# Optimization experiments

Measured on AMD Instinct MI355X. Metric: run time of the kernel, lower is better.

The kernel has to match this reference:

```python
import jax, jax.numpy as jnp
import numpy as np

N = 16384
IN_FEATS = 128
HIDDEN = 128
OUT_FEATS = 64


def setup_inputs() -> dict:
    key = jax.random.key(0)
    ks = jax.random.split(key, 8)
    x = jax.random.normal(ks[0], (N, IN_FEATS), dtype=jnp.float32)
    adj = jax.random.uniform(ks[1], (N, N), dtype=jnp.float32)
    def glorot(k, shape):
        lim = 1.0 / np.sqrt(shape[0])
        return jax.random.uniform(k, shape, minval=-lim, maxval=lim, dtype=jnp.float32)
    W1 = glorot(ks[2], (IN_FEATS, HIDDEN))
    b1 = jnp.zeros((HIDDEN,), dtype=jnp.float32)
    W2 = glorot(ks[3], (HIDDEN, OUT_FEATS))
    b2 = jnp.zeros((OUT_FEATS,), dtype=jnp.float32)
    W_out = glorot(ks[4], (OUT_FEATS, 1))
    b_out = jnp.zeros((1,), dtype=jnp.float32)
    return {"x": x, "adj": adj, "W1": W1, "b1": b1, "W2": W2, "b2": b2,
            "W_out": W_out, "b_out": b_out}


def _gcn_layer(x, adj, W, b):
    # support = x @ W ; out = adj @ support + b  (standard GraphConvLayer)
    return adj @ (x @ W) + b


def reference(x, adj, W1, b1, W2, b2, W_out, b_out):
    h = jax.nn.relu(_gcn_layer(x, adj, W1, b1))      # [N, hidden]
    h = _gcn_layer(h, adj, W2, b2)                   # [N, out_feats]
    pooled = h.sum(axis=0)                           # [out_feats] graph readout
    return pooled @ W_out + b_out                    # [1]
```

## Files before the change

kernel.cpp:

```cpp
#include <hip/hip_runtime.h>
#include <hip/hip_bf16.h>
#include <stdint.h>

#define NN   16384
#define FI   128
#define FH   128
#define FO   64

#define BM   32
#define BK   64
#define LDK  72
#define NT   (NN / BK)
#define NPART 2048

typedef float f32x4 __attribute__((ext_vector_type(4)));
typedef short s16x8 __attribute__((ext_vector_type(8)));
typedef short s16x4 __attribute__((ext_vector_type(4)));

__device__ __forceinline__ unsigned short f2bf(float f) {
    union { float f; unsigned u; } v; v.f = f;
    unsigned u = v.u;
    return (unsigned short)((u + 0x7FFFu + ((u >> 16) & 1u)) >> 16);
}

__global__ __launch_bounds__(256) void k1_s1t(const float* __restrict__ x,
                                              const float* __restrict__ W1,
                                              unsigned short* __restrict__ S1T) {
    __shared__ float w1s[FI][FH];
    __shared__ float xs[64][132];

    const int t  = threadIdx.x;
    const int b  = blockIdx.x;
    const int k0 = b * 64;

    float* wflat = &w1s[0][0];
    for (int i = t; i < FI * FH; i += 256) wflat[i] = W1[i];

    #pragma unroll
    for (int s = 0; s < 8; ++s) {
        int idx = t + 256 * s;
        int r   = idx >> 5;
        int f4  = idx & 31;
        f32x4 vv = *(const f32x4*)(x + (size_t)(k0 + r) * FI + f4 * 4);
        *(f32x4*)(&xs[r][f4 * 4]) = vv;
    }
    __syncthreads();

    const int w = t >> 6;
    const int l = t & 63;

    float acc[32];
    #pragma unroll
    for (int j = 0; j < 32; ++j) acc[j] = 0.f;

    for (int f4 = 0; f4 < 32; ++f4) {
        f32x4 xv = *(const f32x4*)(&xs[l][f4 * 4]);
        #pragma unroll
        for (int e = 0; e < 4; ++e) {
            const int f = f4 * 4 + e;
            #pragma unroll
            for (int cth = 0; cth < 8; ++cth) {
                f32x4 wv = *(const f32x4*)(&w1s[f][w * 32 + cth * 4]);
                acc[cth * 4 + 0] += xv[e] * wv[0];
                acc[cth * 4 + 1] += xv[e] * wv[1];
                acc[cth * 4 + 2] += xv[e] * wv[2];
                acc[cth * 4 + 3] += xv[e] * wv[3];
            }
        }
    }

    const int k = k0 + l;
    #pragma unroll
    for (int j = 0; j < 32; ++j) {
        const int n = w * 32 + j;
        S1T[(size_t)n * NN + k] = f2bf(acc[j]);
    }
}

__global__ __launch_bounds__(256, 2) void k2_agg(const float* __restrict__ adj,
                                                 const unsigned short* __restrict__ S1T,
                                                 float* __restrict__ T,
                                                 float* __restrict__ cpart) {
    __shared__ unsigned short aA[2][BM][LDK];
    __shared__ unsigned short bB[2][FH][LDK];

    const int  t    = threadIdx.x;
    const long m0   = (long)blockIdx.x * BM;
    const int  w    = t >> 6;
    const int  l    = t & 63;
    const int  ar   = t >> 4;
    const int  ac4  = t & 15;
    const int  sn   = t >> 3;
    const int  sch  = t & 7;
    const int  m    = l & 15;
    const int  quad = l >> 4;

    f32x4 acc[2][2];
    #pragma unroll
    for (int i = 0; i < 2; ++i)
        #pragma unroll
        for (int j = 0; j < 2; ++j) acc[i][j] = (f32x4){0.f, 0.f, 0.f, 0.f};

    f32x4 paA0, paA1, paB0, paB1;
    s16x8 psA[4], psB[4];

#define SYNC() do {                                                               \
    asm volatile("s_waitcnt lgkmcnt(0)" ::: "memory");                            \
    __builtin_amdgcn_s_barrier();                                                 \
} while (0)

#define LOAD_TILE(PA0, PA1, PS, KT) do {                                          \
    const long koff_ = (long)(KT) * BK;                                           \
    PA0 = *(const f32x4*)(adj + (m0 + ar) * NN + koff_ + ac4 * 4);                \
    PA1 = *(const f32x4*)(adj + (m0 + ar + 16) * NN + koff_ + ac4 * 4);           \
    _Pragma("unroll")                                                             \
    for (int s_ = 0; s_ < 4; ++s_)                                                \
        PS[s_] = *(const s16x8*)(S1T + (size_t)(sn + 32 * s_) * NN + koff_ + sch * 8); \
} while (0)

#define STAGE(SB, PA0, PA1, PS, KCOL) do {                                        \
    s16x4 q0_, q1_;                                                               \
    _Pragma("unroll")                                                             \
    for (int j_ = 0; j_ < 4; ++j_) {                                              \
        q0_[j_] = (short)f2bf(PA0[j_]);                                           \
        q1_[j_] = (short)f2bf(PA1[j_]);                                           \
    }                                                                             \
    *(s16x4*)(&aA[SB][ar][ac4 * 4])      = q0_;                                   \
    *(s16x4*)(&aA[SB][ar + 16][ac4 * 4]) = q1_;                                   \
    _Pragma("unroll")                                                             \
    for (int s_ = 0; s_ < 4; ++s_)                                                \
        *(s16x8*)(&bB[SB][sn + 32 * s_][sch * 8]) = PS[s_];                       \
      \
      \
      \
    f32x4 pv_;                                                                    \
    _Pragma("unroll")                                                             \
    for (int j_ = 0; j_ < 4; ++j_) {                                              \
        float p_ = PA0[j_] + PA1[j_];                                             \
        p_ += __shfl_xor(p_, 16);                                                 \
        p_ += __shfl_xor(p_, 32);                                                 \
        pv_[j_] = p_;                                                             \
    }                                                                             \
    if (l < 16)                                                                   \
        *(f32x4*)(&cpart[((size_t)blockIdx.x * 4 + w) * NN + (KCOL) + l * 4]) = pv_; \
} while (0)

#define COMPUTE(SB) do {                                                          \
    _Pragma("unroll")                                                             \
    for (int ks = 0; ks < 2; ++ks) {                                              \
        s16x8 af_[2], bf_[2];                                                     \
        _Pragma("unroll")                                                         \
        for (int mt = 0; mt < 2; ++mt)                                            \
            af_[mt] = *(const s16x8*)(&aA[SB][mt * 16 + m][ks * 32 + quad * 8]);  \
        _Pragma("unroll")                                                         \
        for (int nt = 0; nt < 2; ++nt)                                            \
            bf_[nt] = *(const s16x8*)(&bB[SB][w * 32 + nt * 16 + m][ks * 32 + quad * 8]); \
        _Pragma("unroll")                                                         \
        for (int mt = 0; mt < 2; ++mt)                                            \
            _Pragma("unroll")                                                     \
            for (int nt = 0; nt < 2; ++nt)                                        \
                acc[mt][nt] = __builtin_amdgcn_mfma_f32_16x16x32_bf16(            \
                    af_[mt], bf_[nt], acc[mt][nt], 0, 0, 0);                      \
    }                                                                             \
} while (0)

    LOAD_TILE(paA0, paA1, psA, 0);
    LOAD_TILE(paB0, paB1, psB, 1);
    STAGE(0, paA0, paA1, psA, 0);
    SYNC();

    for (int kt2 = 0; kt2 < NT; kt2 += 2) {
        if (kt2 + 2 < NT) LOAD_TILE(paA0, paA1, psA, kt2 + 2);
        COMPUTE(0);
        STAGE(1, paB0, paB1, psB, (kt2 + 1) * BK);
        SYNC();

        if (kt2 + 3 < NT) LOAD_TILE(paB0, paB1, psB, kt2 + 3);
        COMPUTE(1);
        if (kt2 + 2 < NT) STAGE(0, paA0, paA1, psA, (kt2 + 2) * BK);
        SYNC();
    }

#undef LOAD_TILE
#undef STAGE
#undef COMPUTE
#undef SYNC

    #pragma unroll
    for (int mt = 0; mt < 2; ++mt)
        #pragma unroll
        for (int nt = 0; nt < 2; ++nt) {
            const int col = w * 32 + nt * 16 + m;
            #pragma unroll
            for (int r = 0; r < 4; ++r) {
                const long row = m0 + mt * 16 + quad * 4 + r;
                T[row * FH + col] = acc[mt][nt][r];
            }
        }
}

__global__ __launch_bounds__(256) void k3_v(const float* __restrict__ T,
                                            const float* __restrict__ cpart,
                                            const float* __restrict__ b1,
                                            float* __restrict__ v) {
    __shared__ float vp[FH];
    __shared__ float cw[4][64];
    __shared__ float cloc[64];

    const int t = threadIdx.x;
    const int b = blockIdx.x;
    const int w = t >> 6;
    const int l = t & 63;

    float s = 0.f;
    #pragma unroll 8
    for (int i = 0; i < NPART / 4; ++i)
        s += cpart[(size_t)(w + 4 * i) * NN + b * 64 + l];
    cw[w][l] = s;
    if (t < FH) vp[t] = 0.f;
    __syncthreads();
    if (t < 64) cloc[t] = cw[0][t] + cw[1][t] + cw[2][t] + cw[3][t];
    __syncthreads();

    const int kk = t >> 2;
    const int mq = t & 3;
    const int k  = b * 64 + kk;
    const float ck = cloc[kk];

    #pragma unroll
    for (int j4 = 0; j4 < 8; ++j4) {
        f32x4 tv = *(const f32x4*)(T + (size_t)k * FH + mq * 32 + j4 * 4);
        f32x4 bv = *(const f32x4*)(b1 + mq * 32 + j4 * 4);
        #pragma unroll
        for (int e = 0; e < 4; ++e) {
            float h = tv[e] + bv[e];
            h = h > 0.f ? h : 0.f;
            atomicAdd(&vp[mq * 32 + j4 * 4 + e], ck * h);
        }
    }
    __syncthreads();
    if (t < FH) atomicAdd(&v[t], vp[t]);
}

__global__ void k4_out(const float* __restrict__ v, const float* __restrict__ W2,
                       const float* __restrict__ b2, const float* __restrict__ Wout,
                       const float* __restrict__ bout, float* __restrict__ out) {
    const int j = threadIdx.x;
    float pj = (float)NN * b2[j];
    for (int mm = 0; mm < FH; ++mm) pj += v[mm] * W2[mm * FO + j];
    float s = pj * Wout[j];
    #pragma unroll
    for (int off = 32; off; off >>= 1) s += __shfl_down(s, off);
    if (j == 0) out[0] = s + bout[0];
}

extern "C" void kernel_launch(void* const* d_in, const int* in_sizes, int n_in,
                              void* d_out, int out_size, void* d_ws, size_t ws_size,
                              hipStream_t stream) {
    const float* x    = (const float*)d_in[0];
    const float* adj  = (const float*)d_in[1];
    const float* W1   = (const float*)d_in[2];
    const float* b1   = (const float*)d_in[3];
    const float* W2   = (const float*)d_in[4];
    const float* b2   = (const float*)d_in[5];
    const float* Wout = (const float*)d_in[6];
    const float* bout = (const float*)d_in[7];
    float* out = (float*)d_out;

    char* ws = (char*)d_ws;
    unsigned short* S1T = (unsigned short*)ws;
    float* T     = (float*)(ws + (4u   << 20));
    float* cpart = (float*)(ws + (12u  << 20));
    float* v     = (float*)(ws + (140u << 20));

    hipMemsetAsync(v, 0, 512, stream);

    k1_s1t<<<256, 256, 0, stream>>>(x, W1, S1T);
    k2_agg<<<512, 256, 0, stream>>>(adj, S1T, T, cpart);
    k3_v  <<<256, 256, 0, stream>>>(T, cpart, b1, v);
    k4_out<<<1, 64, 0, stream>>>(v, W2, b2, Wout, bout, out);
}
```

Measured before the change: 1.527 ms.

## Halve aggregation row tile, load S1T fragments directly into registers, reduce column partials in LDS

The adjacency aggregation kernel moves from 32-row to 16-row tiles, doubling the grid to 1024 blocks and raising the occupancy hint to 4. Each wave now loads its bf16 S1T MFMA fragments straight from global memory into registers, so the LDS staging buffer for S1T is gone. The per-wave column-sum partials are combined in LDS and written once per block, which halves the cpart array. The cost is that the S1T operand is now fetched once per 16 rows instead of once per 32, doubling its global/L2 traffic.

```diff
diff --git a/kernel.cpp b/kernel.cpp
--- a/kernel.cpp
+++ b/kernel.cpp
@@ -7,11 +7,12 @@
 #define FH   128
 #define FO   64
 
-#define BM   32
+#define BM   16
 #define BK   64
 #define LDK  72
 #define NT   (NN / BK)
-#define NPART 2048
+#define NBLK (NN / BM)
+#define NPART NBLK
 
 typedef float f32x4 __attribute__((ext_vector_type(4)));
 typedef short s16x8 __attribute__((ext_vector_type(8)));
@@ -77,12 +78,12 @@
     }
 }
 
-__global__ __launch_bounds__(256, 2) void k2_agg(const float* __restrict__ adj,
+__global__ __launch_bounds__(256, 4) void k2_agg(const float* __restrict__ adj,
                                                  const unsigned short* __restrict__ S1T,
                                                  float* __restrict__ T,
                                                  float* __restrict__ cpart) {
     __shared__ unsigned short aA[2][BM][LDK];
-    __shared__ unsigned short bB[2][FH][LDK];
+    __shared__ float cs[2][4][BK];
 
     const int  t    = threadIdx.x;
     const long m0   = (long)blockIdx.x * BM;
@@ -90,113 +91,107 @@
     const int  l    = t & 63;
     const int  ar   = t >> 4;
     const int  ac4  = t & 15;
-    const int  sn   = t >> 3;
-    const int  sch  = t & 7;
     const int  m    = l & 15;
     const int  quad = l >> 4;
 
-    f32x4 acc[2][2];
-    #pragma unroll
-    for (int i = 0; i < 2; ++i)
-        #pragma unroll
-        for (int j = 0; j < 2; ++j) acc[i][j] = (f32x4){0.f, 0.f, 0.f, 0.f};
-
-    f32x4 paA0, paA1, paB0, paB1;
-    s16x8 psA[4], psB[4];
+    f32x4 acc[2];
+    acc[0] = (f32x4){0.f, 0.f, 0.f, 0.f};
+    acc[1] = (f32x4){0.f, 0.f, 0.f, 0.f};
+
+    f32x4 paA, paB;
+    s16x8 bfA[2][2], bfB[2][2];
 
 #define SYNC() do {                                                               \
     asm volatile("s_waitcnt lgkmcnt(0)" ::: "memory");                            \
     __builtin_amdgcn_s_barrier();                                                 \
 } while (0)
 
-#define LOAD_TILE(PA0, PA1, PS, KT) do {                                          \
-    const long koff_ = (long)(KT) * BK;                                           \
-    PA0 = *(const f32x4*)(adj + (m0 + ar) * NN + koff_ + ac4 * 4);                \
-    PA1 = *(const f32x4*)(adj + (m0 + ar + 16) * NN + koff_ + ac4 * 4);           \
-    _Pragma("unroll")                                                             \
-    for (int s_ = 0; s_ < 4; ++s_)                                                \
-        PS[s_] = *(const s16x8*)(S1T + (size_t)(sn + 32 * s_) * NN + koff_ + sch * 8); \
-} while (0)
-
-#define STAGE(SB, PA0, PA1, PS, KCOL) do {                                        \
-    s16x4 q0_, q1_;                                                               \
+#define LOADA(PA, KT)                                                             \
+    PA = *(const f32x4*)(adj + (m0 + ar) * NN + (long)(KT) * BK + ac4 * 4)
+
+#define LOADB(BF, KT) do {                                                        \
+    const long ko_ = (long)(KT) * BK;                                             \
+    _Pragma("unroll")                                                             \
+    for (int nt_ = 0; nt_ < 2; ++nt_)                                             \
+        _Pragma("unroll")                                                         \
+        for (int ks_ = 0; ks_ < 2; ++ks_)                                         \
+            BF[nt_][ks_] = *(const s16x8*)(                                       \
+                S1T + (size_t)(w * 32 + nt_ * 16 + m) * NN + ko_ + ks_ * 32 + quad * 8); \
+} while (0)
+
+#define STAGE(SB, PA) do {                                                        \
+    s16x4 q_;                                                                     \
+    _Pragma("unroll")                                                             \
+    for (int j_ = 0; j_ < 4; ++j_) q_[j_] = (short)f2bf(PA[j_]);                  \
+    *(s16x4*)(&aA[SB][ar][ac4 * 4]) = q_;                                         \
+       \
+    f32x4 pv_;                                                                    \
     _Pragma("unroll")                                                             \
     for (int j_ = 0; j_ < 4; ++j_) {                                              \
-        q0_[j_] = (short)f2bf(PA0[j_]);                                           \
-        q1_[j_] = (short)f2bf(PA1[j_]);                                           \
-    }                                                                             \
-    *(s16x4*)(&aA[SB][ar][ac4 * 4])      = q0_;                                   \
-    *(s16x4*)(&aA[SB][ar + 16][ac4 * 4]) = q1_;                                   \
-    _Pragma("unroll")                                                             \
-    for (int s_ = 0; s_ < 4; ++s_)                                                \
-        *(s16x8*)(&bB[SB][sn + 32 * s_][sch * 8]) = PS[s_];                       \
-      \
-      \
-      \
-    f32x4 pv_;                                                                    \
-    _Pragma("unroll")                                                             \
-    for (int j_ = 0; j_ < 4; ++j_) {                                              \
-        float p_ = PA0[j_] + PA1[j_];                                             \
+        float p_ = PA[j_];                                                        \
         p_ += __shfl_xor(p_, 16);                                                 \
         p_ += __shfl_xor(p_, 32);                                                 \
         pv_[j_] = p_;                                                             \
     }                                                                             \
-    if (l < 16)                                                                   \
-        *(f32x4*)(&cpart[((size_t)blockIdx.x * 4 + w) * NN + (KCOL) + l * 4]) = pv_; \
-} while (0)
-
-#define COMPUTE(SB) do {                                                          \
+    if (l < 16) *(f32x4*)(&cs[SB][w][l * 4]) = pv_;                               \
+} while (0)
+
+#define FLUSH(SB, KCOL) do {                                                      \
+    if (t < BK)                                                                   \
+        cpart[(size_t)blockIdx.x * NN + (KCOL) + t] =                             \
+            cs[SB][0][t] + cs[SB][1][t] + cs[SB][2][t] + cs[SB][3][t];            \
+} while (0)
+
+#define COMPUTE(SB, BF) do {                                                      \
     _Pragma("unroll")                                                             \
     for (int ks = 0; ks < 2; ++ks) {                                              \
-        s16x8 af_[2], bf_[2];                                                     \
-        _Pragma("unroll")                                                         \
-        for (int mt = 0; mt < 2; ++mt)                                            \
-            af_[mt] = *(const s16x8*)(&aA[SB][mt * 16 + m][ks * 32 + quad * 8]);  \
+        s16x8 af_ = *(const s16x8*)(&aA[SB][m][ks * 32 + quad * 8]);              \
         _Pragma("unroll")                                                         \
         for (int nt = 0; nt < 2; ++nt)                                            \
-            bf_[nt] = *(const s16x8*)(&bB[SB][w * 32 + nt * 16 + m][ks * 32 + quad * 8]); \
-        _Pragma("unroll")                                                         \
-        for (int mt = 0; mt < 2; ++mt)                                            \
-            _Pragma("unroll")                                                     \
-            for (int nt = 0; nt < 2; ++nt)                                        \
-                acc[mt][nt] = __builtin_amdgcn_mfma_f32_16x16x32_bf16(            \
-                    af_[mt], bf_[nt], acc[mt][nt], 0, 0, 0);                      \
+            acc[nt] = __builtin_amdgcn_mfma_f32_16x16x32_bf16(                    \
+                af_, BF[nt][ks], acc[nt], 0, 0, 0);                               \
     }                                                                             \
 } while (0)
 
-    LOAD_TILE(paA0, paA1, psA, 0);
-    LOAD_TILE(paB0, paB1, psB, 1);
-    STAGE(0, paA0, paA1, psA, 0);
+    LOADA(paA, 0);
+    LOADA(paB, 1);
+    LOADB(bfA, 0);
+    LOADB(bfB, 1);
+    STAGE(0, paA);
     SYNC();
 
     for (int kt2 = 0; kt2 < NT; kt2 += 2) {
-        if (kt2 + 2 < NT) LOAD_TILE(paA0, paA1, psA, kt2 + 2);
-        COMPUTE(0);
-        STAGE(1, paB0, paB1, psB, (kt2 + 1) * BK);
+        if (kt2 + 2 < NT) LOADA(paA, kt2 + 2);
+        FLUSH(0, kt2 * BK);
+        COMPUTE(0, bfA);
+        if (kt2 + 2 < NT) LOADB(bfA, kt2 + 2);
+        STAGE(1, paB);
         SYNC();
 
-        if (kt2 + 3 < NT) LOAD_TILE(paB0, paB1, psB, kt2 + 3);
-        COMPUTE(1);
-        if (kt2 + 2 < NT) STAGE(0, paA0, paA1, psA, (kt2 + 2) * BK);
+        if (kt2 + 3 < NT) LOADA(paB, kt2 + 3);
+        FLUSH(1, (kt2 + 1) * BK);
+        COMPUTE(1, bfB);
+        if (kt2 + 3 < NT) LOADB(bfB, kt2 + 3);
+        if (kt2 + 2 < NT) STAGE(0, paA);
         SYNC();
     }
 
-#undef LOAD_TILE
+#undef LOADA
+#undef LOADB
 #undef STAGE
+#undef FLUSH
 #undef COMPUTE
 #undef SYNC
 
     #pragma unroll
-    for (int mt = 0; mt < 2; ++mt)
+    for (int nt = 0; nt < 2; ++nt) {
+        const int col = w * 32 + nt * 16 + m;
         #pragma unroll
-        for (int nt = 0; nt < 2; ++nt) {
-            const int col = w * 32 + nt * 16 + m;
-            #pragma unroll
-            for (int r = 0; r < 4; ++r) {
-                const long row = m0 + mt * 16 + quad * 4 + r;
-                T[row * FH + col] = acc[mt][nt][r];
-            }
+        for (int r = 0; r < 4; ++r) {
+            const long row = m0 + quad * 4 + r;
+            T[row * FH + col] = acc[nt][r];
         }
+    }
 }
 
 __global__ __launch_bounds__(256) void k3_v(const float* __restrict__ T,
@@ -269,14 +264,14 @@
 
     char* ws = (char*)d_ws;
     unsigned short* S1T = (unsigned short*)ws;
-    float* T     = (float*)(ws + (4u   << 20));
-    float* cpart = (float*)(ws + (12u  << 20));
-    float* v     = (float*)(ws + (140u << 20));
+    float* T     = (float*)(ws + (4u  << 20));
+    float* cpart = (float*)(ws + (12u << 20));
+    float* v     = (float*)(ws + (76u << 20));
 
     hipMemsetAsync(v, 0, 512, stream);
 
     k1_s1t<<<256, 256, 0, stream>>>(x, W1, S1T);
-    k2_agg<<<512, 256, 0, stream>>>(adj, S1T, T, cpart);
+    k2_agg<<<NBLK, 256, 0, stream>>>(adj, S1T, T, cpart);
     k3_v  <<<256, 256, 0, stream>>>(T, cpart, b1, v);
     k4_out<<<1, 64, 0, stream>>>(v, W2, b2, Wout, bout, out);
 }
```

Result: slower. 1.679 ms (+10.0%).

## Split K across two blocks and reduce column sums in LDS before writing

Applied to the files above, without the earlier changes.

The aggregation kernel now splits the K dimension in half, launching twice as many blocks, with each writing a partial T. The final kernel sums the two partials. Column-sum partials are reduced across the four waves in shared memory before being stored, which shrinks the cpart buffer and the reduction work in k3 by 4x. The B tile is single-buffered and occupancy is raised to 4 blocks per CU, at the cost of extra barriers and an extra partial-T write and read.

```diff
diff --git a/kernel.cpp b/kernel.cpp
--- a/kernel.cpp
+++ b/kernel.cpp
@@ -10,8 +10,9 @@
 #define BM   32
 #define BK   64
 #define LDK  72
-#define NT   (NN / BK)
-#define NPART 2048
+#define KHALF (NN / 2)
+#define NTH  (KHALF / BK)
+#define NPART 512
 
 typedef float f32x4 __attribute__((ext_vector_type(4)));
 typedef short s16x8 __attribute__((ext_vector_type(8)));
@@ -77,15 +78,19 @@
     }
 }
 
-__global__ __launch_bounds__(256, 2) void k2_agg(const float* __restrict__ adj,
+__global__ __launch_bounds__(256, 4) void k2_agg(const float* __restrict__ adj,
                                                  const unsigned short* __restrict__ S1T,
-                                                 float* __restrict__ T,
+                                                 float* __restrict__ Tpart,
                                                  float* __restrict__ cpart) {
     __shared__ unsigned short aA[2][BM][LDK];
-    __shared__ unsigned short bB[2][FH][LDK];
+    __shared__ unsigned short bBs[FH][LDK];
+    __shared__ float cs[4][BK];
 
     const int  t    = threadIdx.x;
-    const long m0   = (long)blockIdx.x * BM;
+    const int  rb   = blockIdx.x >> 1;
+    const int  kh   = blockIdx.x & 1;
+    const long m0   = (long)rb * BM;
+    const long k0   = (long)kh * KHALF;
     const int  w    = t >> 6;
     const int  l    = t & 63;
     const int  ar   = t >> 4;
@@ -101,16 +106,16 @@
         #pragma unroll
         for (int j = 0; j < 2; ++j) acc[i][j] = (f32x4){0.f, 0.f, 0.f, 0.f};
 
-    f32x4 paA0, paA1, paB0, paB1;
-    s16x8 psA[4], psB[4];
-
-#define SYNC() do {                                                               \
+    f32x4 paX0, paX1, paY0, paY1;
+    s16x8 psX[4], psY[4];
+
+#define BAR() do {                                                                \
     asm volatile("s_waitcnt lgkmcnt(0)" ::: "memory");                            \
     __builtin_amdgcn_s_barrier();                                                 \
 } while (0)
 
-#define LOAD_TILE(PA0, PA1, PS, KT) do {                                          \
-    const long koff_ = (long)(KT) * BK;                                           \
+#define LOAD(PA0, PA1, PS, J) do {                                                \
+    const long koff_ = k0 + (long)(J) * BK;                                       \
     PA0 = *(const f32x4*)(adj + (m0 + ar) * NN + koff_ + ac4 * 4);                \
     PA1 = *(const f32x4*)(adj + (m0 + ar + 16) * NN + koff_ + ac4 * 4);           \
     _Pragma("unroll")                                                             \
@@ -118,7 +123,16 @@
         PS[s_] = *(const s16x8*)(S1T + (size_t)(sn + 32 * s_) * NN + koff_ + sch * 8); \
 } while (0)
 
-#define STAGE(SB, PA0, PA1, PS, KCOL) do {                                        \
+#define CSUM_STAGEA(SB, PA0, PA1) do {                                            \
+    f32x4 pv_;                                                                    \
+    _Pragma("unroll")                                                             \
+    for (int j_ = 0; j_ < 4; ++j_) {                                              \
+        float p_ = PA0[j_] + PA1[j_];                                             \
+        p_ += __shfl_xor(p_, 16);                                                 \
+        p_ += __shfl_xor(p_, 32);                                                 \
+        pv_[j_] = p_;                                                             \
+    }                                                                             \
+    if (l < 16) *(f32x4*)(&cs[w][l * 4]) = pv_;                                   \
     s16x4 q0_, q1_;                                                               \
     _Pragma("unroll")                                                             \
     for (int j_ = 0; j_ < 4; ++j_) {                                              \
@@ -127,22 +141,18 @@
     }                                                                             \
     *(s16x4*)(&aA[SB][ar][ac4 * 4])      = q0_;                                   \
     *(s16x4*)(&aA[SB][ar + 16][ac4 * 4]) = q1_;                                   \
+} while (0)
+
+#define STAGEB(PS) do {                                                           \
     _Pragma("unroll")                                                             \
     for (int s_ = 0; s_ < 4; ++s_)                                                \
-        *(s16x8*)(&bB[SB][sn + 32 * s_][sch * 8]) = PS[s_];                       \
-      \
-      \
-      \
-    f32x4 pv_;                                                                    \
-    _Pragma("unroll")                                                             \
-    for (int j_ = 0; j_ < 4; ++j_) {                                              \
-        float p_ = PA0[j_] + PA1[j_];                                             \
-        p_ += __shfl_xor(p_, 16);                                                 \
-        p_ += __shfl_xor(p_, 32);                                                 \
-        pv_[j_] = p_;                                                             \
-    }                                                                             \
-    if (l < 16)                                                                   \
-        *(f32x4*)(&cpart[((size_t)blockIdx.x * 4 + w) * NN + (KCOL) + l * 4]) = pv_; \
+        *(s16x8*)(&bBs[sn + 32 * s_][sch * 8]) = PS[s_];                          \
+} while (0)
+
+#define FLUSH(J) do {                                                             \
+    if (t < BK)                                                                   \
+        cpart[(size_t)rb * NN + k0 + (long)(J) * BK + t] =                        \
+            cs[0][t] + cs[1][t] + cs[2][t] + cs[3][t];                            \
 } while (0)
 
 #define COMPUTE(SB) do {                                                          \
@@ -154,7 +164,7 @@
             af_[mt] = *(const s16x8*)(&aA[SB][mt * 16 + m][ks * 32 + quad * 8]);  \
         _Pragma("unroll")                                                         \
         for (int nt = 0; nt < 2; ++nt)                                            \
-            bf_[nt] = *(const s16x8*)(&bB[SB][w * 32 + nt * 16 + m][ks * 32 + quad * 8]); \
+            bf_[nt] = *(const s16x8*)(&bBs[w * 32 + nt * 16 + m][ks * 32 + quad * 8]); \
         _Pragma("unroll")                                                         \
         for (int mt = 0; mt < 2; ++mt)                                            \
             _Pragma("unroll")                                                     \
@@ -164,28 +174,42 @@
     }                                                                             \
 } while (0)
 
-    LOAD_TILE(paA0, paA1, psA, 0);
-    LOAD_TILE(paB0, paB1, psB, 1);
-    STAGE(0, paA0, paA1, psA, 0);
-    SYNC();
-
-    for (int kt2 = 0; kt2 < NT; kt2 += 2) {
-        if (kt2 + 2 < NT) LOAD_TILE(paA0, paA1, psA, kt2 + 2);
+    LOAD(paX0, paX1, psX, 0);
+    LOAD(paY0, paY1, psY, 1);
+    CSUM_STAGEA(0, paX0, paX1);
+    STAGEB(psX);
+    BAR();
+    FLUSH(0);
+    BAR();
+
+    for (int j = 0; j < NTH; j += 2) {
+        if (j + 2 < NTH) LOAD(paX0, paX1, psX, j + 2);
         COMPUTE(0);
-        STAGE(1, paB0, paB1, psB, (kt2 + 1) * BK);
-        SYNC();
-
-        if (kt2 + 3 < NT) LOAD_TILE(paB0, paB1, psB, kt2 + 3);
+        CSUM_STAGEA(1, paY0, paY1);
+        BAR();
+        STAGEB(psY);
+        FLUSH(j + 1);
+        BAR();
+
+        if (j + 3 < NTH) LOAD(paY0, paY1, psY, j + 3);
         COMPUTE(1);
-        if (kt2 + 2 < NT) STAGE(0, paA0, paA1, psA, (kt2 + 2) * BK);
-        SYNC();
-    }
-
-#undef LOAD_TILE
-#undef STAGE
+        if (j + 2 < NTH) CSUM_STAGEA(0, paX0, paX1);
+        BAR();
+        if (j + 2 < NTH) {
+            STAGEB(psX);
+            FLUSH(j + 2);
+        }
+        BAR();
+    }
+
+#undef BAR
+#undef LOAD
+#undef CSUM_STAGEA
+#undef STAGEB
+#undef FLUSH
 #undef COMPUTE
-#undef SYNC
-
+
+    float* Tp = Tpart + (size_t)kh * NN * FH;
     #pragma unroll
     for (int mt = 0; mt < 2; ++mt)
         #pragma unroll
@@ -194,12 +218,12 @@
             #pragma unroll
             for (int r = 0; r < 4; ++r) {
                 const long row = m0 + mt * 16 + quad * 4 + r;
-                T[row * FH + col] = acc[mt][nt][r];
+                Tp[row * FH + col] = acc[mt][nt][r];
             }
         }
 }
 
-__global__ __launch_bounds__(256) void k3_v(const float* __restrict__ T,
+__global__ __launch_bounds__(256) void k3_v(const float* __restrict__ Tpart,
                                             const float* __restrict__ cpart,
                                             const float* __restrict__ b1,
                                             float* __restrict__ v) {
@@ -229,11 +253,12 @@
 
     #pragma unroll
     for (int j4 = 0; j4 < 8; ++j4) {
-        f32x4 tv = *(const f32x4*)(T + (size_t)k * FH + mq * 32 + j4 * 4);
+        f32x4 t0 = *(const f32x4*)(Tpart + (size_t)k * FH + mq * 32 + j4 * 4);
+        f32x4 t1 = *(const f32x4*)(Tpart + ((size_t)NN + k) * FH + mq * 32 + j4 * 4);
         f32x4 bv = *(const f32x4*)(b1 + mq * 32 + j4 * 4);
         #pragma unroll
         for (int e = 0; e < 4; ++e) {
-            float h = tv[e] + bv[e];
+            float h = t0[e] + t1[e] + bv[e];
             h = h > 0.f ? h : 0.f;
             atomicAdd(&vp[mq * 32 + j4 * 4 + e], ck * h);
         }
@@ -269,14 +294,14 @@
 
     char* ws = (char*)d_ws;
     unsigned short* S1T = (unsigned short*)ws;
-    float* T     = (float*)(ws + (4u   << 20));
-    float* cpart = (float*)(ws + (12u  << 20));
-    float* v     = (float*)(ws + (140u << 20));
+    float* Tpart = (float*)(ws + (4u  << 20));
+    float* cpart = (float*)(ws + (20u << 20));
+    float* v     = (float*)(ws + (52u << 20));
 
     hipMemsetAsync(v, 0, 512, stream);
 
     k1_s1t<<<256, 256, 0, stream>>>(x, W1, S1T);
-    k2_agg<<<512, 256, 0, stream>>>(adj, S1T, T, cpart);
-    k3_v  <<<256, 256, 0, stream>>>(T, cpart, b1, v);
+    k2_agg<<<1024, 256, 0, stream>>>(adj, S1T, Tpart, cpart);
+    k3_v  <<<256, 256, 0, stream>>>(Tpart, cpart, b1, v);
     k4_out<<<1, 64, 0, stream>>>(v, W2, b2, Wout, bout, out);
 }
```

After: 1.487 ms. 1.03x faster.
